# Kernel tuning notes

Measured on AMD Instinct MI355X. Metric: run time of the kernel, lower is better.

Reference implementation:

```python
import jax, jax.numpy as jnp
import numpy as np

N, E, X_DIM, EA_DIM, HID, NL, NC, NGRAPH = 50000, 800000, 64, 16, 64, 3, 10, 64
BN_EPS = 1e-5
STD_EPS = 1e-5


def setup_inputs() -> dict:
    key = jax.random.key(0)
    ks = jax.random.split(key, 24)
    w = lambda k, sh: (jax.random.normal(k, sh, jnp.float32) * 0.05)
    inp = {
        'x': jax.random.normal(ks[0], (N, X_DIM), jnp.float32),
        'edge_index': jax.random.randint(ks[1], (2, E), 0, N),
        'batch': jnp.sort(jax.random.randint(ks[2], (N,), 0, NGRAPH)),
        'edge_attr': jax.random.normal(ks[3], (E, EA_DIM), jnp.float32),
        # node / edge encoders
        'node_w': w(ks[4], (X_DIM, HID)), 'node_b': jnp.zeros((HID,), jnp.float32),
        'edge_w': w(ks[5], (EA_DIM, HID)), 'edge_b': jnp.zeros((HID,), jnp.float32),
        # per-layer PNA post_nn Linear(12*3*HID -> HID) and BatchNorm
        'conv_w': w(ks[6], (NL, 12 * 3 * HID, HID)), 'conv_b': jnp.zeros((NL, HID), jnp.float32),
        'bn_g': jnp.ones((NL, HID), jnp.float32), 'bn_b': jnp.zeros((NL, HID), jnp.float32),
        # fc_out: HID -> HID/2 -> HID/4 -> NC
        'fc1_w': w(ks[7], (HID, HID // 2)), 'fc1_b': jnp.zeros((HID // 2,), jnp.float32),
        'fc2_w': w(ks[8], (HID // 2, HID // 4)), 'fc2_b': jnp.zeros((HID // 4,), jnp.float32),
        'fc3_w': w(ks[9], (HID // 4, NC)), 'fc3_b': jnp.zeros((NC,), jnp.float32),
    }
    return inp


def _pna_layer(x, src, dst, ea, deg, degc, log_deg, avg_log, w, b):
    # message: concat([x_i, x_j, edge_attr]) with x_i = x[dst], x_j = x[src]  -> [E, 3H]
    h = jnp.concatenate([x[dst], x[src], ea], axis=-1)
    inv = (1.0 / degc)[:, None]
    s1 = jax.ops.segment_sum(h, dst, num_segments=N)
    mean = s1 * inv
    mean_sq = jax.ops.segment_sum(h * h, dst, num_segments=N) * inv
    std = jnp.sqrt(jax.nn.relu(mean_sq - mean * mean) + STD_EPS)
    has = (deg > 0)[:, None]
    mx = jax.ops.segment_max(h, dst, num_segments=N)
    mx = jnp.where(has, mx, 0.0)
    mn = -jax.ops.segment_max(-h, dst, num_segments=N)
    mn = jnp.where(has, mn, 0.0)
    out = jnp.concatenate([mean, mn, mx, std], axis=-1)  # [N, 4*3H]
    amp = (log_deg / avg_log)[:, None]
    att = (avg_log / log_deg)[:, None]
    out = jnp.concatenate([out, out * amp, out * att], axis=-1)  # [N, 12*3H]
    return out @ w + b


def reference(x, edge_index, batch, edge_attr, node_w, node_b, edge_w, edge_b,
              conv_w, conv_b, bn_g, bn_b, fc1_w, fc1_b, fc2_w, fc2_b, fc3_w, fc3_b):
    src, dst = edge_index[0], edge_index[1]
    x = x @ node_w + node_b
    ea = edge_attr @ edge_w + edge_b
    deg = jax.ops.segment_sum(jnp.ones((E,), jnp.float32), dst, num_segments=N)
    degc = jnp.maximum(deg, 1.0)
    log_deg = jnp.log(degc + 1.0)
    # avg of log(deg+1) over nodes (equivalent to the histogram-based avg_deg['log'])
    avg_log = jnp.mean(jnp.log(deg + 1.0))
    for i in range(NL):
        h = _pna_layer(x, src, dst, ea, deg, degc, log_deg, avg_log, conv_w[i], conv_b[i])
        mu = jnp.mean(h, axis=0)
        var = jnp.mean((h - mu) ** 2, axis=0)  # biased var, as torch BN training mode
        h = (h - mu) * jax.lax.rsqrt(var + BN_EPS) * bn_g[i] + bn_b[i]
        x = jax.nn.relu(h) + x  # dropout is identity in eval
    # global mean pool over graphs
    gsum = jax.ops.segment_sum(x, batch, num_segments=NGRAPH)
    gcnt = jnp.maximum(jax.ops.segment_sum(jnp.ones((N,), jnp.float32), batch, num_segments=NGRAPH), 1.0)
    g = gsum / gcnt[:, None]
    g = jax.nn.relu(g @ fc1_w + fc1_b)
    g = jax.nn.relu(g @ fc2_w + fc2_b)
    return g @ fc3_w + fc3_b
```

## Files before the change

kernel.cpp:

```cpp
#include <hip/hip_runtime.h>
#include <math.h>

#define N_NODES 50000
#define N_EDGES 800000
#define NGRAPH  64
#define KEFF    576

typedef short bf16x8 __attribute__((ext_vector_type(8)));
typedef float f32x4  __attribute__((ext_vector_type(4)));

__device__ inline unsigned short f2bf_rne(float f) {
  unsigned u = __float_as_uint(f);
  unsigned r = u + 0x7FFFu + ((u >> 16) & 1u);
  return (unsigned short)(r >> 16);
}
__device__ inline float bf2f(unsigned short h) {
  return __uint_as_float(((unsigned)h) << 16);
}


__global__ __launch_bounds__(256) void node_enc_kernel(
    const float* __restrict__ xin, const float* __restrict__ nw,
    const float* __restrict__ nb, float* __restrict__ x)
{
  __shared__ float xs[256];
  int tid = threadIdx.x;
  int base = blockIdx.x * 256;
  xs[tid] = xin[base + tid];
  __syncthreads();
  int r = tid >> 6, j = tid & 63;
  float acc = nb[j];
#pragma unroll
  for (int t = 0; t < 64; t++) acc = fmaf(xs[r * 64 + t], nw[t * 64 + j], acc);
  x[base + tid] = acc;
}

__global__ void count_kernel(const int* __restrict__ dst, int* __restrict__ cnt)
{
  int e = blockIdx.x * 256 + threadIdx.x;
  atomicAdd(&cnt[dst[e]], 1);
}

__global__ __launch_bounds__(256) void scan_a_kernel(
    const int* __restrict__ cnt, int* __restrict__ bsum)
{
  __shared__ int s[256];
  int i = blockIdx.x * 256 + threadIdx.x;
  s[threadIdx.x] = (i < N_NODES) ? cnt[i] : 0;
  __syncthreads();
  for (int off = 128; off > 0; off >>= 1) {
    if (threadIdx.x < off) s[threadIdx.x] += s[threadIdx.x + off];
    __syncthreads();
  }
  if (threadIdx.x == 0) bsum[blockIdx.x] = s[0];
}

__global__ __launch_bounds__(256) void scan_b_kernel(
    const int* __restrict__ bsum, int* __restrict__ boff)
{
  __shared__ int s[256];
  int tid = threadIdx.x;
  int v = (tid < 196) ? bsum[tid] : 0;
  s[tid] = v;
  __syncthreads();
  for (int off = 1; off < 256; off <<= 1) {
    int t = (tid >= off) ? s[tid - off] : 0;
    __syncthreads();
    s[tid] += t;
    __syncthreads();
  }
  boff[tid] = s[tid] - v;
}

__global__ __launch_bounds__(256) void scan_c_kernel(
    const int* __restrict__ cnt, const int* __restrict__ boff,
    int* __restrict__ row_ptr)
{
  __shared__ int s[256];
  int tid = threadIdx.x;
  int i = blockIdx.x * 256 + tid;
  int v = (i < N_NODES) ? cnt[i] : 0;
  s[tid] = v;
  __syncthreads();
  for (int off = 1; off < 256; off <<= 1) {
    int t = (tid >= off) ? s[tid - off] : 0;
    __syncthreads();
    s[tid] += t;
    __syncthreads();
  }
  int incl = s[tid];
  int base = boff[blockIdx.x];
  if (i < N_NODES) row_ptr[i] = base + incl - v;
  if (i == N_NODES - 1) row_ptr[N_NODES] = base + incl;
}

__global__ void fill_kernel(const int* __restrict__ src, const int* __restrict__ dst,
                            int* __restrict__ cursor, int* __restrict__ srcs,
                            int* __restrict__ eids)
{
  int e = blockIdx.x * 256 + threadIdx.x;
  int d = dst[e];
  int pos = atomicAdd(&cursor[d], 1);
  srcs[pos] = src[e];
  eids[pos] = e;
}

__global__ __launch_bounds__(256) void deg_log_kernel(
    const int* __restrict__ cnt, float* __restrict__ log_deg,
    double* __restrict__ avgacc)
{
  __shared__ double sb[256];
  int i = blockIdx.x * 256 + threadIdx.x;
  double c = 0.0;
  if (i < N_NODES) {
    int d = cnt[i];
    int dc = d > 0 ? d : 1;
    log_deg[i] = logf((float)dc + 1.0f);
    c = (double)logf((float)d + 1.0f);
  }
  sb[threadIdx.x] = c;
  __syncthreads();
  for (int off = 128; off > 0; off >>= 1) {
    if (threadIdx.x < off) sb[threadIdx.x] += sb[threadIdx.x + off];
    __syncthreads();
  }
  if (threadIdx.x == 0) atomicAdd(avgacc, sb[0]);
}

__global__ void finalize_avg_kernel(const double* __restrict__ avgacc,
                                    float* __restrict__ avgf)
{
  *avgf = (float)(*avgacc / (double)N_NODES);
}

__global__ void gbound_kernel(const int* __restrict__ batch, int* __restrict__ gcnt)
{
  __shared__ int sb[65];
  int g = threadIdx.x;
  int lo = 0, hi = N_NODES;
  while (lo < hi) { int mid = (lo + hi) >> 1; if (batch[mid] < g) lo = mid + 1; else hi = mid; }
  sb[g] = lo;
  if (g == 0) sb[64] = N_NODES;
  __syncthreads();
  gcnt[g] = sb[g + 1] - sb[g];
}


__global__ __launch_bounds__(256) void wprep_kernel(
    const float* __restrict__ conv_w, unsigned short* __restrict__ wh,
    unsigned short* __restrict__ wl)
{
  int idx = blockIdx.x * 256 + threadIdx.x;
  int k = idx % 576;
  int c = (idx / 576) % 192;
  int l = idx / (576 * 192);
  int s = c >> 6, j = c & 63;
  const float* CW = conv_w + (size_t)l * 2304 * 64;
  float v;
  if (k < 64) {
    int base = s * 768 + k;
    v = CW[base * 64 + j] + CW[(base + 192) * 64 + j] + CW[(base + 384) * 64 + j];
  } else {
    const int srcseg[8] = {1, 2, 4, 5, 7, 8, 10, 11};
    int q = (k >> 6) - 1;
    int t = k & 63;
    v = CW[(s * 768 + srcseg[q] * 64 + t) * 64 + j];
  }
  unsigned short hh = f2bf_rne(v);
  wh[idx] = hh;
  wl[idx] = f2bf_rne(v - bf2f(hh));
}

__global__ void bprep_kernel(const float* __restrict__ conv_w, float* __restrict__ beff)
{
  int l = blockIdx.x;
  int s = threadIdx.x >> 6, j = threadIdx.x & 63;
  const float* CW = conv_w + (size_t)l * 2304 * 64 + (size_t)(s * 768 + 576) * 64;
  float sum = 0.f;
#pragma unroll
  for (int t = 0; t < 64; t++) sum += CW[t * 64 + j];
  beff[(l * 3 + s) * 64 + j] = sum * 0.0031622776601683794f;
}


__global__ __launch_bounds__(256) void agg_e_kernel(
    const float* __restrict__ eattr, const float* __restrict__ edge_w,
    const float* __restrict__ edge_b, const int* __restrict__ row_ptr,
    const int* __restrict__ eids,
    unsigned short* __restrict__ agg_h, unsigned short* __restrict__ agg_l)
{
  int lane = threadIdx.x & 63;
  int quad = lane >> 4, a16 = lane & 15;
  int n = blockIdx.x * 4 + (threadIdx.x >> 6);
  if (n >= N_NODES) return;
  float ew[16];
#pragma unroll
  for (int t = 0; t < 16; t++) ew[t] = edge_w[t * 64 + lane];
  float eb = edge_b[lane];
  int s0 = row_ptr[n], s1 = row_ptr[n + 1];
  float se = 0.f, qe = 0.f, mxe = -3.4e38f, mne = 3.4e38f;

  for (int j = s0; j < s1; j += 4) {
    int idx = j + quad;
    float av = 0.f;
    if (idx < s1) av = eattr[(size_t)eids[idx] * 16 + a16];
    unsigned au = __float_as_uint(av);
    float ea[4];
#pragma unroll
    for (int q = 0; q < 4; q++) {
      float c0 = eb, c1 = 0.f;
#pragma unroll
      for (int t = 0; t < 8; t++) {
        c0 = fmaf(__uint_as_float(__builtin_amdgcn_readlane(au, q * 16 + t)), ew[t], c0);
        c1 = fmaf(__uint_as_float(__builtin_amdgcn_readlane(au, q * 16 + 8 + t)), ew[8 + t], c1);
      }
      ea[q] = c0 + c1;
    }
    int rem = s1 - j;
#pragma unroll
    for (int q = 0; q < 4; q++) {
      if (q < rem) {
        se += ea[q]; qe = fmaf(ea[q], ea[q], qe);
        mxe = fmaxf(mxe, ea[q]); mne = fminf(mne, ea[q]);
      }
    }
  }

  int deg = s1 - s0;
  float inv = 1.0f / fmaxf((float)deg, 1.0f);
  bool has = deg > 0;
  float m_e = se * inv, ms_e = qe * inv;
  float sd_e = sqrtf(fmaxf(ms_e - m_e * m_e, 0.f) + 1e-5f);
  float mx_e = has ? mxe : 0.f, mn_e = has ? mne : 0.f;

  unsigned short* bh = agg_h + (size_t)n * KEFF;
  unsigned short* bl = agg_l + (size_t)n * KEFF;
#define W2(off, val) { float _v = (val); unsigned short _h = f2bf_rne(_v); \
                       bh[(off) + lane] = _h; bl[(off) + lane] = f2bf_rne(_v - bf2f(_h)); }
  W2(128, m_e); W2(256, mn_e); W2(384, mx_e); W2(512, sd_e);
#undef W2
}


__global__ __launch_bounds__(256) void agg_x_kernel(
    const float* __restrict__ x, const int* __restrict__ srcs,
    const int* __restrict__ row_ptr,
    unsigned short* __restrict__ agg_h, unsigned short* __restrict__ agg_l)
{
  int lane = threadIdx.x & 63;
  int n = blockIdx.x * 4 + (threadIdx.x >> 6);
  if (n >= N_NODES) return;
  float xd = x[(size_t)n * 64 + lane];
  int s0 = row_ptr[n], s1 = row_ptr[n + 1];
  float sA = 0.f, sB = 0.f, sC = 0.f, sD = 0.f;
  float qA = 0.f, qB = 0.f, qC = 0.f, qD = 0.f;
  float mx0 = -3.4e38f, mx1 = -3.4e38f, mn0 = 3.4e38f, mn1 = 3.4e38f;
  int j = s0;
  for (; j + 3 < s1; j += 4) {
    int e0 = srcs[j], e1 = srcs[j + 1], e2 = srcs[j + 2], e3 = srcs[j + 3];
    float xa = x[(size_t)e0 * 64 + lane];
    float xb = x[(size_t)e1 * 64 + lane];
    float xc = x[(size_t)e2 * 64 + lane];
    float xe = x[(size_t)e3 * 64 + lane];
    sA += xa; sB += xb; sC += xc; sD += xe;
    qA = fmaf(xa, xa, qA); qB = fmaf(xb, xb, qB);
    qC = fmaf(xc, xc, qC); qD = fmaf(xe, xe, qD);
    mx0 = fmaxf(mx0, fmaxf(xa, xb)); mx1 = fmaxf(mx1, fmaxf(xc, xe));
    mn0 = fminf(mn0, fminf(xa, xb)); mn1 = fminf(mn1, fminf(xc, xe));
  }
  for (; j < s1; j++) {
    float xa = x[(size_t)srcs[j] * 64 + lane];
    sA += xa; qA = fmaf(xa, xa, qA);
    mx0 = fmaxf(mx0, xa); mn0 = fminf(mn0, xa);
  }
  float sx = (sA + sB) + (sC + sD);
  float qx = (qA + qB) + (qC + qD);
  float mxx = fmaxf(mx0, mx1), mnx = fminf(mn0, mn1);

  int deg = s1 - s0;
  float inv = 1.0f / fmaxf((float)deg, 1.0f);
  bool has = deg > 0;
  float m_s = sx * inv, ms_s = qx * inv;
  float sd_s = sqrtf(fmaxf(ms_s - m_s * m_s, 0.f) + 1e-5f);
  float mx_s = has ? mxx : 0.f, mn_s = has ? mnx : 0.f;

  unsigned short* bh = agg_h + (size_t)n * KEFF;
  unsigned short* bl = agg_l + (size_t)n * KEFF;
#define W2(off, val) { float _v = (val); unsigned short _h = f2bf_rne(_v); \
                       bh[(off) + lane] = _h; bl[(off) + lane] = f2bf_rne(_v - bf2f(_h)); }
  W2(0,   has ? xd : 0.f);
  W2(64,  m_s); W2(192, mn_s); W2(320, mx_s); W2(448, sd_s);
#undef W2
}


__global__ __launch_bounds__(256, 3) void gemm_kernel(
    const unsigned short* __restrict__ Ah, const unsigned short* __restrict__ Al,
    const unsigned short* __restrict__ Wh, const unsigned short* __restrict__ Wl,
    const float* __restrict__ beff, const float* __restrict__ bias,
    const float* __restrict__ log_deg, const float* __restrict__ avg_ptr,
    float* __restrict__ h, double* __restrict__ bnacc)
{
  __shared__ __align__(16) short AsH[64 * 40], AsL[64 * 40];
  __shared__ __align__(16) short BsH[192 * 40], BsL[192 * 40];
  int tid = threadIdx.x;
  int lane = tid & 63, w = tid >> 6;
  int quad = lane >> 4, l15 = lane & 15;
  int n0 = blockIdx.x * 64;

  int arow = tid >> 2, ac = tid & 3;
  int an = n0 + arow; if (an >= N_NODES) an = N_NODES - 1;
  const unsigned short* gah = Ah + (size_t)an * KEFF + ac * 8;
  const unsigned short* gal = Al + (size_t)an * KEFF + ac * 8;

  f32x4 acc[4][3] = {};

  for (int k0 = 0; k0 < KEFF; k0 += 32) {
    *(float4*)(AsH + arow * 40 + ac * 8) = *(const float4*)(gah + k0);
    *(float4*)(AsL + arow * 40 + ac * 8) = *(const float4*)(gal + k0);
#pragma unroll
    for (int q = 0; q < 6; q++) {
      int r = tid + (q < 3 ? q : q - 3) * 256;
      int col = r >> 2, cc = r & 3;
      const unsigned short* gb = (q < 3) ? Wh : Wl;
      short* bs = (q < 3) ? BsH : BsL;
      *(float4*)(bs + col * 40 + cc * 8) =
          *(const float4*)(gb + (size_t)col * KEFF + k0 + cc * 8);
    }
    __syncthreads();

    bf16x8 bh[3], bl[3];
#pragma unroll
    for (int s = 0; s < 3; s++) {
      int col = s * 64 + w * 16 + l15;
      bh[s] = *(const bf16x8*)(BsH + col * 40 + quad * 8);
      bl[s] = *(const bf16x8*)(BsL + col * 40 + quad * 8);
    }
#pragma unroll
    for (int i = 0; i < 4; i++) {
      int row = i * 16 + l15;
      bf16x8 ah = *(const bf16x8*)(AsH + row * 40 + quad * 8);
      bf16x8 al = *(const bf16x8*)(AsL + row * 40 + quad * 8);
#pragma unroll
      for (int s = 0; s < 3; s++) {
        acc[i][s] = __builtin_amdgcn_mfma_f32_16x16x32_bf16(ah, bh[s], acc[i][s], 0, 0, 0);
        acc[i][s] = __builtin_amdgcn_mfma_f32_16x16x32_bf16(al, bh[s], acc[i][s], 0, 0, 0);
        acc[i][s] = __builtin_amdgcn_mfma_f32_16x16x32_bf16(ah, bl[s], acc[i][s], 0, 0, 0);
      }
    }
    __syncthreads();
  }

  float avg = *avg_ptr;
  int col = w * 16 + l15;
  float be0 = beff[col], be1 = beff[64 + col], be2 = beff[128 + col];
  float bi = bias[col];
  float ss = 0.f, sq = 0.f;
#pragma unroll
  for (int i = 0; i < 4; i++) {
#pragma unroll
    for (int r = 0; r < 4; r++) {
      int n = n0 + i * 16 + quad * 4 + r;
      if (n < N_NODES) {
        float ld = log_deg[n];
        float amp = ld / avg, att = avg / ld;
        float v = (acc[i][0][r] + be0) + amp * (acc[i][1][r] + be1)
                + att * (acc[i][2][r] + be2) + bi;
        h[(size_t)n * 64 + col] = v;
        ss += v; sq = fmaf(v, v, sq);
      }
    }
  }
  ss += __shfl_xor(ss, 16, 64); ss += __shfl_xor(ss, 32, 64);
  sq += __shfl_xor(sq, 16, 64); sq += __shfl_xor(sq, 32, 64);
  if (quad == 0) {
    atomicAdd(&bnacc[col], (double)ss);
    atomicAdd(&bnacc[64 + col], (double)sq);
  }
}


__global__ void bn_finalize_kernel(const double* __restrict__ accS,
                                   const double* __restrict__ accQ,
                                   const float* __restrict__ g,
                                   float* __restrict__ muf, float* __restrict__ scf)
{
  int j = threadIdx.x;
  double mu = accS[j] / (double)N_NODES;
  double var = accQ[j] / (double)N_NODES - mu * mu;
  double rstd = 1.0 / sqrt(var + 1e-5);
  muf[j] = (float)mu;
  scf[j] = (float)(rstd * (double)g[j]);
}

__global__ __launch_bounds__(256) void apply_kernel(
    const float* __restrict__ h, const float* __restrict__ muf,
    const float* __restrict__ scf, const float* __restrict__ bnb,
    float* __restrict__ x)
{
  int i4 = blockIdx.x * 256 + threadIdx.x;
  const float4* h4 = (const float4*)h;
  float4* x4 = (float4*)x;
  int c4 = i4 & 15;
  float4 hv = h4[i4], xv = x4[i4];
  float4 mu = ((const float4*)muf)[c4];
  float4 sc = ((const float4*)scf)[c4];
  float4 bb = ((const float4*)bnb)[c4];
  float4 r;
  r.x = fmaxf((hv.x - mu.x) * sc.x + bb.x, 0.f) + xv.x;
  r.y = fmaxf((hv.y - mu.y) * sc.y + bb.y, 0.f) + xv.y;
  r.z = fmaxf((hv.z - mu.z) * sc.z + bb.z, 0.f) + xv.z;
  r.w = fmaxf((hv.w - mu.w) * sc.w + bb.w, 0.f) + xv.w;
  x4[i4] = r;
}


__global__ __launch_bounds__(256) void pool_kernel(
    const float* __restrict__ x, const int* __restrict__ batch,
    float* __restrict__ gsum)
{
  int tid = threadIdx.x;
  int j = tid & 63, ri = tid >> 6;
  float acc = 0.f; int cur = -1;
  for (int k = 0; k < 16; k++) {
    int n = blockIdx.x * 64 + k * 4 + ri;
    if (n < N_NODES) {
      int b = batch[n];
      if (b != cur) {
        if (cur >= 0) atomicAdd(&gsum[cur * 64 + j], acc);
        cur = b; acc = 0.f;
      }
      acc += x[(size_t)n * 64 + j];
    }
  }
  if (cur >= 0) atomicAdd(&gsum[cur * 64 + j], acc);
}

__global__ void fc_kernel(const float* __restrict__ gsum, const int* __restrict__ gcnt,
                          const float* __restrict__ w1, const float* __restrict__ b1,
                          const float* __restrict__ w2, const float* __restrict__ b2,
                          const float* __restrict__ w3, const float* __restrict__ b3,
                          float* __restrict__ out)
{
  int g = threadIdx.x;
  float cnt = fmaxf((float)gcnt[g], 1.0f);
  float gv[64];
#pragma unroll
  for (int j = 0; j < 64; j++) gv[j] = gsum[g * 64 + j] / cnt;
  float a1[32];
#pragma unroll
  for (int o = 0; o < 32; o++) {
    float s = b1[o];
#pragma unroll
    for (int j = 0; j < 64; j++) s = fmaf(gv[j], w1[j * 32 + o], s);
    a1[o] = fmaxf(s, 0.f);
  }
  float a2[16];
#pragma unroll
  for (int o = 0; o < 16; o++) {
    float s = b2[o];
#pragma unroll
    for (int j = 0; j < 32; j++) s = fmaf(a1[j], w2[j * 16 + o], s);
    a2[o] = fmaxf(s, 0.f);
  }
#pragma unroll
  for (int o = 0; o < 10; o++) {
    float s = b3[o];
#pragma unroll
    for (int j = 0; j < 16; j++) s = fmaf(a2[j], w3[j * 10 + o], s);
    out[g * 10 + o] = s;
  }
}


extern "C" void kernel_launch(void* const* d_in, const int* in_sizes, int n_in,
                              void* d_out, int out_size, void* d_ws, size_t ws_size,
                              hipStream_t stream)
{
  (void)in_sizes; (void)n_in; (void)out_size; (void)ws_size;
  const float* xin    = (const float*)d_in[0];
  const int*   ei     = (const int*)d_in[1];
  const int*   batch  = (const int*)d_in[2];
  const float* eattr  = (const float*)d_in[3];
  const float* node_w = (const float*)d_in[4];
  const float* node_b = (const float*)d_in[5];
  const float* edge_w = (const float*)d_in[6];
  const float* edge_b = (const float*)d_in[7];
  const float* conv_w = (const float*)d_in[8];
  const float* conv_b = (const float*)d_in[9];
  const float* bn_g   = (const float*)d_in[10];
  const float* bn_b   = (const float*)d_in[11];
  const float* fc1_w  = (const float*)d_in[12];
  const float* fc1_b  = (const float*)d_in[13];
  const float* fc2_w  = (const float*)d_in[14];
  const float* fc2_b  = (const float*)d_in[15];
  const float* fc3_w  = (const float*)d_in[16];
  const float* fc3_b  = (const float*)d_in[17];
  float* out = (float*)d_out;
  const int* srcp = ei;
  const int* dstp = ei + N_EDGES;

  char* p = (char*)d_ws;
  auto alloc = [&](size_t b) { char* r = p; p += (b + 255) & ~(size_t)255; return (void*)r; };
  float*  x       = (float*)alloc((size_t)N_NODES * 64 * 4);
  float*  h       = (float*)alloc((size_t)N_NODES * 64 * 4);
  unsigned short* agg_h = (unsigned short*)alloc((size_t)N_NODES * KEFF * 2);
  unsigned short* agg_l = (unsigned short*)alloc((size_t)N_NODES * KEFF * 2);
  unsigned short* wh    = (unsigned short*)alloc((size_t)3 * 192 * KEFF * 2);
  unsigned short* wl    = (unsigned short*)alloc((size_t)3 * 192 * KEFF * 2);
  int*    srcs    = (int*)alloc((size_t)N_EDGES * 4);
  int*    eids    = (int*)alloc((size_t)N_EDGES * 4);
  float*  beff    = (float*)alloc((size_t)3 * 3 * 64 * 4);
  int*    row_ptr = (int*)alloc((N_NODES + 1) * 4);
  int*    cursor  = (int*)alloc((size_t)N_NODES * 4);
  int*    cnt     = (int*)alloc((size_t)N_NODES * 4);
  float*  log_deg = (float*)alloc((size_t)N_NODES * 4);
  int*    bsum    = (int*)alloc(256 * 4);
  int*    boff    = (int*)alloc(256 * 4);
  double* avgacc  = (double*)alloc(256);
  float*  avgf    = (float*)alloc(256);
  double* bnacc   = (double*)alloc(3 * 128 * 8);
  float*  muf     = (float*)alloc(256);
  float*  scf     = (float*)alloc(256);
  float*  gsum    = (float*)alloc((size_t)NGRAPH * 64 * 4);
  int*    gcnt    = (int*)alloc((size_t)NGRAPH * 4);

  hipMemsetAsync(cnt, 0, (size_t)N_NODES * 4, stream);
  hipMemsetAsync(avgacc, 0, 8, stream);
  hipMemsetAsync(gsum, 0, (size_t)NGRAPH * 64 * 4, stream);
  hipMemsetAsync(bnacc, 0, 3 * 128 * 8, stream);

  node_enc_kernel<<<12500, 256, 0, stream>>>(xin, node_w, node_b, x);
  count_kernel<<<3125, 256, 0, stream>>>(dstp, cnt);
  scan_a_kernel<<<196, 256, 0, stream>>>(cnt, bsum);
  scan_b_kernel<<<1, 256, 0, stream>>>(bsum, boff);
  scan_c_kernel<<<196, 256, 0, stream>>>(cnt, boff, row_ptr);
  hipMemcpyAsync(cursor, row_ptr, (size_t)N_NODES * 4, hipMemcpyDeviceToDevice, stream);
  fill_kernel<<<3125, 256, 0, stream>>>(srcp, dstp, cursor, srcs, eids);
  deg_log_kernel<<<196, 256, 0, stream>>>(cnt, log_deg, avgacc);
  finalize_avg_kernel<<<1, 1, 0, stream>>>(avgacc, avgf);
  gbound_kernel<<<1, 64, 0, stream>>>(batch, gcnt);
  wprep_kernel<<<1296, 256, 0, stream>>>(conv_w, wh, wl);
  bprep_kernel<<<3, 192, 0, stream>>>(conv_w, beff);

  agg_e_kernel<<<12500, 256, 0, stream>>>(eattr, edge_w, edge_b, row_ptr,
                                          eids, agg_h, agg_l);

  for (int l = 0; l < 3; l++) {
    agg_x_kernel<<<12500, 256, 0, stream>>>(x, srcs, row_ptr, agg_h, agg_l);
    gemm_kernel<<<782, 256, 0, stream>>>(agg_h, agg_l,
                                         wh + (size_t)l * 192 * KEFF,
                                         wl + (size_t)l * 192 * KEFF,
                                         beff + l * 192, conv_b + l * 64,
                                         log_deg, avgf, h, bnacc + l * 128);
    bn_finalize_kernel<<<1, 64, 0, stream>>>(bnacc + l * 128, bnacc + l * 128 + 64,
                                             bn_g + l * 64, muf, scf);
    apply_kernel<<<3125, 256, 0, stream>>>(h, muf, scf, bn_b + l * 64, x);
  }

  pool_kernel<<<782, 256, 0, stream>>>(x, batch, gsum);
  fc_kernel<<<1, 64, 0, stream>>>(gsum, gcnt, fc1_w, fc1_b, fc2_w, fc2_b,
                                  fc3_w, fc3_b, out);
}
```

Before: 706.4 us.

## Compute edge encoder on MFMA with split-bf16 and unroll gather loop by eight

The per-node edge aggregation now projects each node's incoming edge attributes with MFMA 16x16x32 bf16 instructions. It uses a three-term hi/lo split to approximate fp32 accuracy, replacing the readlane-based scalar FMA loop that handled four edges per iteration. Sixteen edges are processed per tile and reduced across quads with shuffles. The x-gather aggregation loop is also unrolled to eight outstanding loads for more memory-level parallelism. The split-bf16 product uses truncation rather than rounding and drops the lo*lo term, so results may differ slightly; low-degree nodes waste part of each 16-edge tile.

```diff
diff --git a/kernel.cpp b/kernel.cpp
--- a/kernel.cpp
+++ b/kernel.cpp
@@ -9,6 +9,8 @@
 typedef short bf16x8 __attribute__((ext_vector_type(8)));
 typedef float f32x4  __attribute__((ext_vector_type(4)));
 
+union U8 { bf16x8 v; unsigned u[4]; };
+
 __device__ inline unsigned short f2bf_rne(float f) {
   unsigned u = __float_as_uint(f);
   unsigned r = u + 0x7FFFu + ((u >> 16) & 1u);
@@ -16,6 +18,22 @@
 }
 __device__ inline float bf2f(unsigned short h) {
   return __uint_as_float(((unsigned)h) << 16);
+}
+
+__device__ inline void split8(const float* a, bf16x8& H, bf16x8& L) {
+  U8 hh, ll;
+#pragma unroll
+  for (int p = 0; p < 4; p++) {
+    unsigned u0 = __float_as_uint(a[2 * p]);
+    unsigned u1 = __float_as_uint(a[2 * p + 1]);
+    unsigned h0 = u0 & 0xFFFF0000u, h1 = u1 & 0xFFFF0000u;
+    hh.u[p] = (h0 >> 16) | h1;
+    float r0 = a[2 * p] - __uint_as_float(h0);
+    float r1 = a[2 * p + 1] - __uint_as_float(h1);
+    ll.u[p] = ((__float_as_uint(r0) & 0xFFFF0000u) >> 16)
+            | (__float_as_uint(r1) & 0xFFFF0000u);
+  }
+  H = hh.v; L = ll.v;
 }
 
 
@@ -190,48 +208,85 @@
     unsigned short* __restrict__ agg_h, unsigned short* __restrict__ agg_l)
 {
   int lane = threadIdx.x & 63;
-  int quad = lane >> 4, a16 = lane & 15;
+  int quad = lane >> 4, l15 = lane & 15;
   int n = blockIdx.x * 4 + (threadIdx.x >> 6);
   if (n >= N_NODES) return;
-  float ew[16];
-#pragma unroll
-  for (int t = 0; t < 16; t++) ew[t] = edge_w[t * 64 + lane];
-  float eb = edge_b[lane];
+
+  bf16x8 Bh[4], Bl[4];
+  float ebc[4];
+#pragma unroll
+  for (int b = 0; b < 4; b++) {
+    float wv[8];
+#pragma unroll
+    for (int j = 0; j < 8; j++) {
+      int k = quad * 8 + j;
+      wv[j] = (k < 16) ? edge_w[k * 64 + b * 16 + l15] : 0.f;
+    }
+    split8(wv, Bh[b], Bl[b]);
+    ebc[b] = edge_b[b * 16 + l15];
+  }
+
   int s0 = row_ptr[n], s1 = row_ptr[n + 1];
-  float se = 0.f, qe = 0.f, mxe = -3.4e38f, mne = 3.4e38f;
-
-  for (int j = s0; j < s1; j += 4) {
-    int idx = j + quad;
-    float av = 0.f;
-    if (idx < s1) av = eattr[(size_t)eids[idx] * 16 + a16];
-    unsigned au = __float_as_uint(av);
-    float ea[4];
-#pragma unroll
-    for (int q = 0; q < 4; q++) {
-      float c0 = eb, c1 = 0.f;
-#pragma unroll
-      for (int t = 0; t < 8; t++) {
-        c0 = fmaf(__uint_as_float(__builtin_amdgcn_readlane(au, q * 16 + t)), ew[t], c0);
-        c1 = fmaf(__uint_as_float(__builtin_amdgcn_readlane(au, q * 16 + 8 + t)), ew[8 + t], c1);
+  int deg = s1 - s0;
+  float sum[4] = {}, sq[4] = {};
+  float mx[4] = {-3.4e38f, -3.4e38f, -3.4e38f, -3.4e38f};
+  float mn[4] = {3.4e38f, 3.4e38f, 3.4e38f, 3.4e38f};
+
+  for (int t0 = s0; t0 < s1; t0 += 16) {
+    int pos = t0 + l15;
+    if (pos >= s1) pos = s1 - 1;
+    int eid = eids[pos];
+    bf16x8 Ah, Al;
+    if (quad < 2) {
+      float a[8];
+      const float4* ap = (const float4*)(eattr + (size_t)eid * 16 + quad * 8);
+      float4 f0 = ap[0], f1 = ap[1];
+      a[0] = f0.x; a[1] = f0.y; a[2] = f0.z; a[3] = f0.w;
+      a[4] = f1.x; a[5] = f1.y; a[6] = f1.z; a[7] = f1.w;
+      split8(a, Ah, Al);
+    } else {
+      U8 z; z.u[0] = z.u[1] = z.u[2] = z.u[3] = 0;
+      Ah = z.v; Al = z.v;
+    }
+    f32x4 C[4] = {};
+#pragma unroll
+    for (int b = 0; b < 4; b++) {
+      C[b] = __builtin_amdgcn_mfma_f32_16x16x32_bf16(Ah, Bh[b], C[b], 0, 0, 0);
+      C[b] = __builtin_amdgcn_mfma_f32_16x16x32_bf16(Al, Bh[b], C[b], 0, 0, 0);
+      C[b] = __builtin_amdgcn_mfma_f32_16x16x32_bf16(Ah, Bl[b], C[b], 0, 0, 0);
+    }
+#pragma unroll
+    for (int r = 0; r < 4; r++) {
+      bool rv = (t0 + quad * 4 + r) < s1;
+#pragma unroll
+      for (int b = 0; b < 4; b++) {
+        float v = C[b][r] + ebc[b];
+        float vm = rv ? v : 0.f;
+        sum[b] += vm; sq[b] = fmaf(vm, vm, sq[b]);
+        mx[b] = fmaxf(mx[b], v); mn[b] = fminf(mn[b], v);
       }
-      ea[q] = c0 + c1;
-    }
-    int rem = s1 - j;
-#pragma unroll
-    for (int q = 0; q < 4; q++) {
-      if (q < rem) {
-        se += ea[q]; qe = fmaf(ea[q], ea[q], qe);
-        mxe = fmaxf(mxe, ea[q]); mne = fminf(mne, ea[q]);
-      }
-    }
-  }
-
-  int deg = s1 - s0;
+    }
+  }
+
+#pragma unroll
+  for (int b = 0; b < 4; b++) {
+    sum[b] += __shfl_xor(sum[b], 16, 64); sum[b] += __shfl_xor(sum[b], 32, 64);
+    sq[b]  += __shfl_xor(sq[b], 16, 64);  sq[b]  += __shfl_xor(sq[b], 32, 64);
+    mx[b] = fmaxf(mx[b], __shfl_xor(mx[b], 16, 64));
+    mx[b] = fmaxf(mx[b], __shfl_xor(mx[b], 32, 64));
+    mn[b] = fminf(mn[b], __shfl_xor(mn[b], 16, 64));
+    mn[b] = fminf(mn[b], __shfl_xor(mn[b], 32, 64));
+  }
+  float S  = quad == 0 ? sum[0] : quad == 1 ? sum[1] : quad == 2 ? sum[2] : sum[3];
+  float Q  = quad == 0 ? sq[0]  : quad == 1 ? sq[1]  : quad == 2 ? sq[2]  : sq[3];
+  float MX = quad == 0 ? mx[0]  : quad == 1 ? mx[1]  : quad == 2 ? mx[2]  : mx[3];
+  float MN = quad == 0 ? mn[0]  : quad == 1 ? mn[1]  : quad == 2 ? mn[2]  : mn[3];
+
   float inv = 1.0f / fmaxf((float)deg, 1.0f);
   bool has = deg > 0;
-  float m_e = se * inv, ms_e = qe * inv;
+  float m_e = S * inv, ms_e = Q * inv;
   float sd_e = sqrtf(fmaxf(ms_e - m_e * m_e, 0.f) + 1e-5f);
-  float mx_e = has ? mxe : 0.f, mn_e = has ? mne : 0.f;
+  float mx_e = has ? MX : 0.f, mn_e = has ? MN : 0.f;
 
   unsigned short* bh = agg_h + (size_t)n * KEFF;
   unsigned short* bl = agg_l + (size_t)n * KEFF;
@@ -256,17 +311,39 @@
   float qA = 0.f, qB = 0.f, qC = 0.f, qD = 0.f;
   float mx0 = -3.4e38f, mx1 = -3.4e38f, mn0 = 3.4e38f, mn1 = 3.4e38f;
   int j = s0;
+  for (; j + 7 < s1; j += 8) {
+    int e0 = srcs[j],     e1 = srcs[j + 1], e2 = srcs[j + 2], e3 = srcs[j + 3];
+    int e4 = srcs[j + 4], e5 = srcs[j + 5], e6 = srcs[j + 6], e7 = srcs[j + 7];
+    float x0 = x[(size_t)e0 * 64 + lane];
+    float x1 = x[(size_t)e1 * 64 + lane];
+    float x2 = x[(size_t)e2 * 64 + lane];
+    float x3 = x[(size_t)e3 * 64 + lane];
+    float x4 = x[(size_t)e4 * 64 + lane];
+    float x5 = x[(size_t)e5 * 64 + lane];
+    float x6 = x[(size_t)e6 * 64 + lane];
+    float x7 = x[(size_t)e7 * 64 + lane];
+    sA += x0; sB += x1; sC += x2; sD += x3;
+    sA += x4; sB += x5; sC += x6; sD += x7;
+    qA = fmaf(x0, x0, qA); qB = fmaf(x1, x1, qB);
+    qC = fmaf(x2, x2, qC); qD = fmaf(x3, x3, qD);
+    qA = fmaf(x4, x4, qA); qB = fmaf(x5, x5, qB);
+    qC = fmaf(x6, x6, qC); qD = fmaf(x7, x7, qD);
+    mx0 = fmaxf(mx0, fmaxf(fmaxf(x0, x1), fmaxf(x2, x3)));
+    mx1 = fmaxf(mx1, fmaxf(fmaxf(x4, x5), fmaxf(x6, x7)));
+    mn0 = fminf(mn0, fminf(fminf(x0, x1), fminf(x2, x3)));
+    mn1 = fminf(mn1, fminf(fminf(x4, x5), fminf(x6, x7)));
+  }
   for (; j + 3 < s1; j += 4) {
     int e0 = srcs[j], e1 = srcs[j + 1], e2 = srcs[j + 2], e3 = srcs[j + 3];
-    float xa = x[(size_t)e0 * 64 + lane];
-    float xb = x[(size_t)e1 * 64 + lane];
-    float xc = x[(size_t)e2 * 64 + lane];
-    float xe = x[(size_t)e3 * 64 + lane];
-    sA += xa; sB += xb; sC += xc; sD += xe;
-    qA = fmaf(xa, xa, qA); qB = fmaf(xb, xb, qB);
-    qC = fmaf(xc, xc, qC); qD = fmaf(xe, xe, qD);
-    mx0 = fmaxf(mx0, fmaxf(xa, xb)); mx1 = fmaxf(mx1, fmaxf(xc, xe));
-    mn0 = fminf(mn0, fminf(xa, xb)); mn1 = fminf(mn1, fminf(xc, xe));
+    float x0 = x[(size_t)e0 * 64 + lane];
+    float x1 = x[(size_t)e1 * 64 + lane];
+    float x2 = x[(size_t)e2 * 64 + lane];
+    float x3 = x[(size_t)e3 * 64 + lane];
+    sA += x0; sB += x1; sC += x2; sD += x3;
+    qA = fmaf(x0, x0, qA); qB = fmaf(x1, x1, qB);
+    qC = fmaf(x2, x2, qC); qD = fmaf(x3, x3, qD);
+    mx0 = fmaxf(mx0, fmaxf(x0, x1)); mx1 = fmaxf(mx1, fmaxf(x2, x3));
+    mn0 = fminf(mn0, fminf(x0, x1)); mn1 = fminf(mn1, fminf(x2, x3));
   }
   for (; j < s1; j++) {
     float xa = x[(size_t)srcs[j] * 64 + lane];
```

New measurement: 694.0 us. Within noise of the previous version (-1.8%).

## Load GEMM fragments directly from global memory and unroll aggregation gather by eight

Applied to the files above, without the earlier changes.

The GEMM kernel stops staging A and B tiles through shared memory and barriers. Each lane now loads its MFMA operand fragments straight from global memory into registers, with the k-loop unrolled by two and the occupancy hint lowered from 3 to 2. Separately, the neighbour-gather loop in agg_x_kernel is unrolled to eight loads in flight per iteration to expose more memory-level parallelism. The direct loads drop LDS traffic and synchronisation but read the same A and W data redundantly across waves, relying on L1/L2 to absorb it, and they raise register pressure.

```diff
diff --git a/kernel.cpp b/kernel.cpp
--- a/kernel.cpp
+++ b/kernel.cpp
@@ -256,17 +256,39 @@
   float qA = 0.f, qB = 0.f, qC = 0.f, qD = 0.f;
   float mx0 = -3.4e38f, mx1 = -3.4e38f, mn0 = 3.4e38f, mn1 = 3.4e38f;
   int j = s0;
+  for (; j + 7 < s1; j += 8) {
+    int e0 = srcs[j],     e1 = srcs[j + 1], e2 = srcs[j + 2], e3 = srcs[j + 3];
+    int e4 = srcs[j + 4], e5 = srcs[j + 5], e6 = srcs[j + 6], e7 = srcs[j + 7];
+    float x0 = x[(size_t)e0 * 64 + lane];
+    float x1 = x[(size_t)e1 * 64 + lane];
+    float x2 = x[(size_t)e2 * 64 + lane];
+    float x3 = x[(size_t)e3 * 64 + lane];
+    float x4 = x[(size_t)e4 * 64 + lane];
+    float x5 = x[(size_t)e5 * 64 + lane];
+    float x6 = x[(size_t)e6 * 64 + lane];
+    float x7 = x[(size_t)e7 * 64 + lane];
+    sA += x0; sB += x1; sC += x2; sD += x3;
+    sA += x4; sB += x5; sC += x6; sD += x7;
+    qA = fmaf(x0, x0, qA); qB = fmaf(x1, x1, qB);
+    qC = fmaf(x2, x2, qC); qD = fmaf(x3, x3, qD);
+    qA = fmaf(x4, x4, qA); qB = fmaf(x5, x5, qB);
+    qC = fmaf(x6, x6, qC); qD = fmaf(x7, x7, qD);
+    mx0 = fmaxf(mx0, fmaxf(fmaxf(x0, x1), fmaxf(x2, x3)));
+    mx1 = fmaxf(mx1, fmaxf(fmaxf(x4, x5), fmaxf(x6, x7)));
+    mn0 = fminf(mn0, fminf(fminf(x0, x1), fminf(x2, x3)));
+    mn1 = fminf(mn1, fminf(fminf(x4, x5), fminf(x6, x7)));
+  }
   for (; j + 3 < s1; j += 4) {
     int e0 = srcs[j], e1 = srcs[j + 1], e2 = srcs[j + 2], e3 = srcs[j + 3];
-    float xa = x[(size_t)e0 * 64 + lane];
-    float xb = x[(size_t)e1 * 64 + lane];
-    float xc = x[(size_t)e2 * 64 + lane];
-    float xe = x[(size_t)e3 * 64 + lane];
-    sA += xa; sB += xb; sC += xc; sD += xe;
-    qA = fmaf(xa, xa, qA); qB = fmaf(xb, xb, qB);
-    qC = fmaf(xc, xc, qC); qD = fmaf(xe, xe, qD);
-    mx0 = fmaxf(mx0, fmaxf(xa, xb)); mx1 = fmaxf(mx1, fmaxf(xc, xe));
-    mn0 = fminf(mn0, fminf(xa, xb)); mn1 = fminf(mn1, fminf(xc, xe));
+    float x0 = x[(size_t)e0 * 64 + lane];
+    float x1 = x[(size_t)e1 * 64 + lane];
+    float x2 = x[(size_t)e2 * 64 + lane];
+    float x3 = x[(size_t)e3 * 64 + lane];
+    sA += x0; sB += x1; sC += x2; sD += x3;
+    qA = fmaf(x0, x0, qA); qB = fmaf(x1, x1, qB);
+    qC = fmaf(x2, x2, qC); qD = fmaf(x3, x3, qD);
+    mx0 = fmaxf(mx0, fmaxf(x0, x1)); mx1 = fmaxf(mx1, fmaxf(x2, x3));
+    mn0 = fminf(mn0, fminf(x0, x1)); mn1 = fminf(mn1, fminf(x2, x3));
   }
   for (; j < s1; j++) {
     float xa = x[(size_t)srcs[j] * 64 + lane];
@@ -294,61 +316,61 @@
 }
 
 
-__global__ __launch_bounds__(256, 3) void gemm_kernel(
+__global__ __launch_bounds__(256, 2) void gemm_kernel(
     const unsigned short* __restrict__ Ah, const unsigned short* __restrict__ Al,
     const unsigned short* __restrict__ Wh, const unsigned short* __restrict__ Wl,
     const float* __restrict__ beff, const float* __restrict__ bias,
     const float* __restrict__ log_deg, const float* __restrict__ avg_ptr,
     float* __restrict__ h, double* __restrict__ bnacc)
 {
-  __shared__ __align__(16) short AsH[64 * 40], AsL[64 * 40];
-  __shared__ __align__(16) short BsH[192 * 40], BsL[192 * 40];
   int tid = threadIdx.x;
   int lane = tid & 63, w = tid >> 6;
   int quad = lane >> 4, l15 = lane & 15;
   int n0 = blockIdx.x * 64;
 
-  int arow = tid >> 2, ac = tid & 3;
-  int an = n0 + arow; if (an >= N_NODES) an = N_NODES - 1;
-  const unsigned short* gah = Ah + (size_t)an * KEFF + ac * 8;
-  const unsigned short* gal = Al + (size_t)an * KEFF + ac * 8;
+  const unsigned short* pah[4];
+  const unsigned short* pal[4];
+#pragma unroll
+  for (int i = 0; i < 4; i++) {
+    int an = n0 + i * 16 + l15;
+    if (an >= N_NODES) an = N_NODES - 1;
+    pah[i] = Ah + (size_t)an * KEFF;
+    pal[i] = Al + (size_t)an * KEFF;
+  }
+  const unsigned short* pbh[3];
+  const unsigned short* pbl[3];
+#pragma unroll
+  for (int s = 0; s < 3; s++) {
+    int col = s * 64 + w * 16 + l15;
+    pbh[s] = Wh + (size_t)col * KEFF;
+    pbl[s] = Wl + (size_t)col * KEFF;
+  }
 
   f32x4 acc[4][3] = {};
 
+#pragma unroll 2
   for (int k0 = 0; k0 < KEFF; k0 += 32) {
-    *(float4*)(AsH + arow * 40 + ac * 8) = *(const float4*)(gah + k0);
-    *(float4*)(AsL + arow * 40 + ac * 8) = *(const float4*)(gal + k0);
-#pragma unroll
-    for (int q = 0; q < 6; q++) {
-      int r = tid + (q < 3 ? q : q - 3) * 256;
-      int col = r >> 2, cc = r & 3;
-      const unsigned short* gb = (q < 3) ? Wh : Wl;
-      short* bs = (q < 3) ? BsH : BsL;
-      *(float4*)(bs + col * 40 + cc * 8) =
-          *(const float4*)(gb + (size_t)col * KEFF + k0 + cc * 8);
-    }
-    __syncthreads();
-
-    bf16x8 bh[3], bl[3];
+    int ko = k0 + quad * 8;
+    bf16x8 ahf[4], alf[4], bhf[3], blf[3];
+#pragma unroll
+    for (int i = 0; i < 4; i++) {
+      ahf[i] = *(const bf16x8*)(pah[i] + ko);
+      alf[i] = *(const bf16x8*)(pal[i] + ko);
+    }
 #pragma unroll
     for (int s = 0; s < 3; s++) {
-      int col = s * 64 + w * 16 + l15;
-      bh[s] = *(const bf16x8*)(BsH + col * 40 + quad * 8);
-      bl[s] = *(const bf16x8*)(BsL + col * 40 + quad * 8);
+      bhf[s] = *(const bf16x8*)(pbh[s] + ko);
+      blf[s] = *(const bf16x8*)(pbl[s] + ko);
     }
 #pragma unroll
     for (int i = 0; i < 4; i++) {
-      int row = i * 16 + l15;
-      bf16x8 ah = *(const bf16x8*)(AsH + row * 40 + quad * 8);
-      bf16x8 al = *(const bf16x8*)(AsL + row * 40 + quad * 8);
 #pragma unroll
       for (int s = 0; s < 3; s++) {
-        acc[i][s] = __builtin_amdgcn_mfma_f32_16x16x32_bf16(ah, bh[s], acc[i][s], 0, 0, 0);
-        acc[i][s] = __builtin_amdgcn_mfma_f32_16x16x32_bf16(al, bh[s], acc[i][s], 0, 0, 0);
-        acc[i][s] = __builtin_amdgcn_mfma_f32_16x16x32_bf16(ah, bl[s], acc[i][s], 0, 0, 0);
+        acc[i][s] = __builtin_amdgcn_mfma_f32_16x16x32_bf16(ahf[i], bhf[s], acc[i][s], 0, 0, 0);
+        acc[i][s] = __builtin_amdgcn_mfma_f32_16x16x32_bf16(alf[i], bhf[s], acc[i][s], 0, 0, 0);
+        acc[i][s] = __builtin_amdgcn_mfma_f32_16x16x32_bf16(ahf[i], blf[s], acc[i][s], 0, 0, 0);
       }
     }
-    __syncthreads();
   }
 
   float avg = *avg_ptr;
```

Measured after the change: 911.0 us. +29.0%, slower.
